# Kernel tuning notes

Measured on AMD Instinct MI355X. Metric: run time of the kernel, lower is better.

The kernel has to match this reference:

```python
import jax, jax.numpy as jnp
import numpy as np

EPS = 1e-5
LEAK = 0.01  # PADLoC uses ABN = BatchNorm + LeakyReLU as norm_act


def bn_act(x, g, b):
    # train-mode batch norm over (B,H,W) + leaky relu
    mu = jnp.mean(x, axis=(0, 2, 3), keepdims=True)
    var = jnp.var(x, axis=(0, 2, 3), keepdims=True)
    y = (x - mu) * jax.lax.rsqrt(var + EPS) * g[None, :, None, None] + b[None, :, None, None]
    return jnp.where(y >= 0, y, LEAK * y)


def depthwise3x3(x, w):
    # x: (B,C,H,W), w: (C,1,3,3), dilation (1,1), padding 1, groups=C
    C = x.shape[1]
    return jax.lax.conv_general_dilated(
        x, w, window_strides=(1, 1), padding=((1, 1), (1, 1)),
        feature_group_count=C, dimension_numbers=('NCHW', 'OIHW', 'NCHW'))


def pointwise(x, w):
    # 1x1 conv, no bias; w: (Cout, Cin)
    return jnp.einsum('bchw,oc->bohw', x, w)


def _gather_vals(x_flat, idx):
    # x_flat: (B,C,P), idx: (B,HW,9) float indices -> (B,C,HW,9)
    B, C, P = x_flat.shape
    i = idx.astype(jnp.int32).reshape(B, -1)  # (B, HW*9)
    out = jax.vmap(lambda xf, ii: xf[:, ii])(x_flat, i)  # (B,C,HW*9)
    return out.reshape(B, C, idx.shape[1], 9)


def setup_inputs() -> dict:
    key = jax.random.key(0)
    ks = jax.random.split(key, 8)
    B, Cin, Cout, H, W = 1, 256, 128, 64, 192
    sc = 0.05
    return {
        'x': jax.random.normal(ks[0], (B, Cin, H, W), jnp.float32),
        'x_range': jax.random.normal(ks[1], (B, 1, H, W), jnp.float32),
        'range_out': jax.random.normal(ks[2], (Cin, 1, 3, 3), jnp.float32) * sc,
        'w_reduce': jax.random.normal(ks[3], (Cout, Cin), jnp.float32) * sc,
        'g_r': jnp.ones((Cout,), jnp.float32), 'b_r': jnp.zeros((Cout,), jnp.float32),
        'dw1': jax.random.normal(ks[4], (Cout, 1, 3, 3), jnp.float32) * sc,
        'pw1': jax.random.normal(ks[5], (Cout, Cout), jnp.float32) * sc,
        'g1': jnp.ones((Cout,), jnp.float32), 'b1': jnp.zeros((Cout,), jnp.float32),
        'dw2': jax.random.normal(ks[6], (Cout, 1, 3, 3), jnp.float32) * sc,
        'pw2': jax.random.normal(ks[7], (Cout, Cout), jnp.float32) * sc,
        'g2': jnp.ones((Cout,), jnp.float32), 'b2': jnp.zeros((Cout,), jnp.float32),
    }


def reference(x, x_range, range_out, w_reduce, g_r, b_r, dw1, pw1, g1, b1, dw2, pw2, g2, b2):
    B, Cin, H, W = x.shape
    Hp, Wp = H + 2, W + 2
    P = Hp * Wp  # flattened padded spatial size
    x_off = jnp.array([-1, 0, 1, -1, 0, 1, -1, 0, 1], jnp.float32)
    y_off = jnp.array([-1, -1, -1, 0, 0, 0, 1, 1, 1], jnp.float32)

    offset = 3.0 * jax.nn.sigmoid(x_range)  # (B,1,H,W)

    # base (undeformed) flattened indices of the 9 taps around each interior pixel
    v = jnp.arange(P, dtype=jnp.float32)[:, None]  # (P,1)
    pre_v = v + x_off + y_off * Wp                 # (P,9)
    pre_v = pre_v.reshape(Hp, Wp, 9)[1:H + 1, 1:W + 1].reshape(-1, 9)  # (HW,9)
    pre_v = jnp.broadcast_to(pre_v[None], (B, H * W, 9))

    # fractional offsets: only x-direction is scaled by offset in _3x3box
    offset_v = offset.reshape(B, H * W, 1) * x_off.reshape(1, 1, 9) + (y_off * Wp).reshape(1, 1, 9)

    x_padded = jnp.pad(x, ((0, 0), (0, 0), (1, 1), (1, 1)))  # (B,C,Hp,Wp)
    clamp = lambda a: jnp.clip(a, 0.0, P - 1.0)

    after_v = pre_v + offset_v
    av_f = clamp(pre_v + jnp.floor(offset_v))
    av_f1 = clamp(av_f + x_off)
    av_c = clamp(pre_v + jnp.ceil(offset_v))
    av_c1 = clamp(av_c + x_off)

    xflat = x_padded.reshape(B, Cin, P)
    vf = _gather_vals(xflat, av_f)
    vf1 = _gather_vals(xflat, av_f1)
    vc = _gather_vals(xflat, av_c)
    vc1 = _gather_vals(xflat, av_c1)

    f1 = jnp.abs(after_v - av_f)[:, None] * vf + jnp.abs(av_f1 - after_v)[:, None] * vf1
    f2 = jnp.abs(after_v - av_c1)[:, None] * vc1 + jnp.abs(av_c - after_v)[:, None] * vc
    interp = (jnp.abs((after_v - av_f) / Wp)[:, None] * f1
              + jnp.abs((av_c1 - after_v) / Wp)[:, None] * f2)  # (B,C,HW,9)

    y = jnp.sum(interp * range_out.reshape(1, Cin, 1, 9), -1).reshape(B, Cin, H, W)
    y = bn_act(pointwise(y, w_reduce), g_r, b_r)
    y = bn_act(pointwise(depthwise3x3(y, dw1), pw1), g1, b1)
    y = bn_act(pointwise(depthwise3x3(y, dw2), pw2), g2, b2)
    return y
```

## Files before the change

### kernel.cpp

```cpp
#include <hip/hip_runtime.h>
#include <hip/hip_bf16.h>

#define HW    12288
#define Wimg  192
#define Himg  64
#define Wpad  194
#define Ppad  12804

static __device__ __forceinline__ unsigned short f2bf(float f) {
    union { float f; unsigned int u; } v; v.f = f;
    unsigned int r = v.u + 0x7fffu + ((v.u >> 16) & 1u);
    return (unsigned short)(r >> 16);
}
static __device__ __forceinline__ float bf2f(unsigned short h) {
    union { unsigned int u; float f; } v; v.u = ((unsigned int)h) << 16;
    return v.f;
}
static __device__ __forceinline__ float bflo(unsigned int u) {
    union { unsigned int u; float f; } v; v.u = u << 16; return v.f;
}
static __device__ __forceinline__ float bfhi(unsigned int u) {
    union { unsigned int u; float f; } v; v.u = u & 0xffff0000u; return v.f;
}

__global__ __launch_bounds__(256, 6) void k_deform(
    const float* __restrict__ x,
    const float* __restrict__ xr,
    const float* __restrict__ rout,
    unsigned short* __restrict__ y0)
{
    __shared__ unsigned short s_x[32][240];

    const int cblk = blockIdx.x;
    const int tile = blockIdx.y;
    const int tid  = threadIdx.x;
    const int pl   = tid & 63;
    const int wv   = __builtin_amdgcn_readfirstlane(tid >> 6);
    const int h    = tile / 3;
    const int w0   = (tile - h * 3) * 64;
    const int w    = w0 + pl;
    const int gp   = h * Wimg + w;

    int   li[6];
    float gw[6][3];
    const float off = 3.0f / (1.0f + expf(-xr[gp]));

    #pragma unroll
    for (int t = 0; t < 6; ++t) {
        const int xo = (t & 1) ? 1 : -1;
        const int yo = (t >> 1) - 1;
        float ov  = off * (float)xo;
        int   iv  = yo * Wpad;
        int   pre = (h + 1) * Wpad + (w + 1) + xo + iv;
        float after = (float)(pre + iv) + ov;
        int fl = (int)floorf(ov);
        int ce = (int)ceilf(ov);
        int av_f  = min(max(pre + fl + iv, 0), Ppad - 1);
        int av_f1 = min(max(av_f + xo,    0), Ppad - 1);
        int av_c  = min(max(pre + ce + iv, 0), Ppad - 1);
        int av_c1 = min(max(av_c + xo,    0), Ppad - 1);
        float wf  = fabsf(after - (float)av_f);
        float wf1 = fabsf((float)av_f1 - after);
        float wc1 = fabsf(after - (float)av_c1);
        float wc  = fabsf((float)av_c - after);
        float s1 = wf  * (1.0f / Wpad);
        float s2 = wc1 * (1.0f / Wpad);
        int   i4[4] = { av_f, av_f1, av_c1, av_c };
        float w4[4] = { s1 * wf, s1 * wf1, s2 * wc1, s2 * wc };
        int b = min(min(i4[0], i4[1]), min(i4[2], i4[3]));
        const int base = (h + 1 + 2 * yo) * Wpad + w0 - 4;
        li[t] = (t >> 1) * 80 + min(max(b - base, 0), 71);
        #pragma unroll
        for (int s = 0; s < 3; ++s) {
            float ws = 0.0f;
            #pragma unroll
            for (int j = 0; j < 4; ++j)
                ws += (i4[j] == b + s) ? w4[j] : 0.0f;
            int av = b + s;
            int r  = av / Wpad;
            int cc = av - r * Wpad;
            bool inb = (r >= 1) && (r <= Himg) && (cc >= 1) && (cc <= Wimg);
            gw[t][s] = inb ? ws : 0.0f;
        }
    }

    const int jj = tid;
    int  xoff = 0;
    bool valid = false;
    int  rr = 0, jcol = 0;
    if (jj < 222) {
        rr   = jj / 74;
        jcol = jj - rr * 74;
        const int flat = (h + 1 + 2 * (rr - 1)) * Wpad + w0 - 4 + jcol;
        if (flat >= 0 && flat < Ppad) {
            const int r = flat / Wpad;
            const int c = flat - r * Wpad;
            valid = (r >= 1) && (r <= Himg) && (c >= 1) && (c <= Wimg);
            xoff  = valid ? ((r - 1) * Wimg + (c - 1)) : 0;
        }
    }
    const float* xb = x + (size_t)(cblk * 32) * HW;
    for (int c = 0; c < 32; ++c) {
        if (jj < 222) {
            float v = valid ? xb[(size_t)c * HW + xoff] : 0.0f;
            s_x[c][rr * 80 + jcol] = f2bf(v);
        }
    }
    __syncthreads();

    const int c0l = wv * 8;
    #pragma unroll 2
    for (int i = 0; i < 8; ++i) {
        const int cl = c0l + i;
        const unsigned short* sxc = s_x[cl];
        const float* rc = rout + (cblk * 32 + cl) * 9;
        float acc = 0.0f;
        #pragma unroll
        for (int t = 0; t < 6; ++t) {
            float part = gw[t][0] * bf2f(sxc[li[t]])
                       + gw[t][1] * bf2f(sxc[li[t] + 1])
                       + gw[t][2] * bf2f(sxc[li[t] + 2]);
            const int k = 3 * (t >> 1) + ((t & 1) ? 2 : 0);
            acc += rc[k] * part;
        }
        y0[(size_t)(cblk * 32 + cl) * HW + gp] = f2bf(acc);
    }
}

template <int CIN>
__global__ __launch_bounds__(256) void k_pw(
    const unsigned short* __restrict__ A,
    const float* __restrict__ Wm,
    unsigned short* __restrict__ Zp0,
    unsigned short* __restrict__ Zp1)
{
    __shared__ float s_a[32][64];
    __shared__ float s_w[32][68];
    const int tid = threadIdx.x;
    const int tx  = tid & 15;
    const int ty  = tid >> 4;
    const int px0 = blockIdx.x * 64;
    const int o0  = blockIdx.y * 64;
    const int KH  = CIN / 2;
    const int cb0 = blockIdx.z * KH;
    unsigned short* __restrict__ Zp = blockIdx.z ? Zp1 : Zp0;

    float acc[4][4];
    #pragma unroll
    for (int i = 0; i < 4; ++i)
        #pragma unroll
        for (int j = 0; j < 4; ++j) acc[i][j] = 0.0f;

    const int arow = tid >> 3;
    const int acg  = tid & 7;
    const int wo = tid >> 5;
    const int wl = tid & 31;

    for (int cb = cb0; cb < cb0 + KH; cb += 32) {
        {
            const uint4* ap = (const uint4*)(A + (size_t)(cb + arow) * HW + px0);
            uint4 u = ap[acg];
            float4 lo = make_float4(bflo(u.x), bfhi(u.x), bflo(u.y), bfhi(u.y));
            float4 hi = make_float4(bflo(u.z), bfhi(u.z), bflo(u.w), bfhi(u.w));
            *(float4*)&s_a[arow][acg * 8]     = lo;
            *(float4*)&s_a[arow][acg * 8 + 4] = hi;
        }
        #pragma unroll
        for (int i = 0; i < 8; ++i)
            s_w[wl][wo + 8 * i] = Wm[(size_t)(o0 + wo + 8 * i) * CIN + cb + wl];
        __syncthreads();
        #pragma unroll
        for (int cc = 0; cc < 32; ++cc) {
            float4 a4 = *(const float4*)&s_a[cc][tx * 4];
            float4 w4 = *(const float4*)&s_w[cc][ty * 4];
            acc[0][0] += w4.x * a4.x; acc[0][1] += w4.x * a4.y;
            acc[0][2] += w4.x * a4.z; acc[0][3] += w4.x * a4.w;
            acc[1][0] += w4.y * a4.x; acc[1][1] += w4.y * a4.y;
            acc[1][2] += w4.y * a4.z; acc[1][3] += w4.y * a4.w;
            acc[2][0] += w4.z * a4.x; acc[2][1] += w4.z * a4.y;
            acc[2][2] += w4.z * a4.z; acc[2][3] += w4.z * a4.w;
            acc[3][0] += w4.w * a4.x; acc[3][1] += w4.w * a4.y;
            acc[3][2] += w4.w * a4.z; acc[3][3] += w4.w * a4.w;
        }
        __syncthreads();
    }

    #pragma unroll
    for (int i = 0; i < 4; ++i) {
        ushort4 v;
        v.x = f2bf(acc[i][0]); v.y = f2bf(acc[i][1]);
        v.z = f2bf(acc[i][2]); v.w = f2bf(acc[i][3]);
        *(ushort4*)&Zp[(size_t)(o0 + ty * 4 + i) * HW + px0 + tx * 4] = v;
    }
}

__global__ __launch_bounds__(256) void k_stats2(
    const unsigned short* __restrict__ Zp0,
    const unsigned short* __restrict__ Zp1,
    float* __restrict__ psum)
{
    __shared__ float s_s[4], s_q[4];
    const int c   = blockIdx.x;
    const int tid = threadIdx.x;
    const size_t base = (size_t)c * HW;
    const uint2* a4 = (const uint2*)(Zp0 + base);
    const uint2* b4 = (const uint2*)(Zp1 + base);
    float s = 0.0f, q = 0.0f;
    #pragma unroll
    for (int i = 0; i < 12; ++i) {
        uint2 a = a4[tid + i * 256];
        uint2 b = b4[tid + i * 256];
        float v0 = bflo(a.x) + bflo(b.x);
        float v1 = bfhi(a.x) + bfhi(b.x);
        float v2 = bflo(a.y) + bflo(b.y);
        float v3 = bfhi(a.y) + bfhi(b.y);
        s += v0 + v1 + v2 + v3;
        q += v0 * v0 + v1 * v1 + v2 * v2 + v3 * v3;
    }
    #pragma unroll
    for (int off = 32; off > 0; off >>= 1) {
        s += __shfl_down(s, off, 64);
        q += __shfl_down(q, off, 64);
    }
    if ((tid & 63) == 0) { s_s[tid >> 6] = s; s_q[tid >> 6] = q; }
    __syncthreads();
    if (tid == 0) {
        psum[2 * c]     = s_s[0] + s_s[1] + s_s[2] + s_s[3];
        psum[2 * c + 1] = s_q[0] + s_q[1] + s_q[2] + s_q[3];
    }
}

__global__ __launch_bounds__(256) void k_dw2(
    const unsigned short* __restrict__ Zp0,
    const unsigned short* __restrict__ Zp1,
    const float* __restrict__ psum,
    const float* __restrict__ g,
    const float* __restrict__ b,
    const float* __restrict__ dwgt,
    ushort4* __restrict__ D)
{
    const int t  = blockIdx.x * 256 + threadIdx.x;
    const int c  = t / 3072;
    const int gg = t - c * 3072;
    const int h  = gg / 48;
    const int w0 = (gg - h * 48) << 2;

    const float s   = psum[2 * c];
    const float q   = psum[2 * c + 1];
    const float mu  = s * (1.0f / HW);
    const float var = q * (1.0f / HW) - mu * mu;
    const float sc  = g[c] * rsqrtf(var + 1e-5f);
    const float sh  = b[c] - mu * sc;

    float wk[9];
    #pragma unroll
    for (int k = 0; k < 9; ++k) wk[k] = dwgt[c * 9 + k];

    const unsigned short* z0 = Zp0 + (size_t)c * HW;
    const unsigned short* z1 = Zp1 + (size_t)c * HW;
    float v[3][6];
    #pragma unroll
    for (int ky = 0; ky < 3; ++ky) {
        const int hh  = h + ky - 1;
        const bool rin = (hh >= 0) && (hh < Himg);
        #pragma unroll
        for (int j = 0; j < 6; ++j) {
            const int ww = w0 - 1 + j;
            const bool in = rin && (ww >= 0) && (ww < Wimg);
            float z = in ? (bf2f(z0[hh * Wimg + ww]) + bf2f(z1[hh * Wimg + ww]))
                         : 0.0f;
            float y = z * sc + sh;
            y = (y >= 0.0f) ? y : 0.01f * y;
            v[ky][j] = in ? y : 0.0f;
        }
    }

    ushort4 o;
    float oo[4];
    #pragma unroll
    for (int j = 0; j < 4; ++j) {
        float a = 0.0f;
        #pragma unroll
        for (int ky = 0; ky < 3; ++ky)
            #pragma unroll
            for (int kx = 0; kx < 3; ++kx)
                a += wk[ky * 3 + kx] * v[ky][j + kx];
        oo[j] = a;
    }
    o.x = f2bf(oo[0]); o.y = f2bf(oo[1]); o.z = f2bf(oo[2]); o.w = f2bf(oo[3]);
    D[t] = o;
}

__global__ __launch_bounds__(256) void k_final2(
    const unsigned short* __restrict__ Zp0,
    const unsigned short* __restrict__ Zp1,
    const float* __restrict__ psum,
    const float* __restrict__ g,
    const float* __restrict__ b,
    float4* __restrict__ out)
{
    const int f = blockIdx.x * 256 + threadIdx.x;
    const int c = f / 3072;

    const float s   = psum[2 * c];
    const float q   = psum[2 * c + 1];
    const float mu  = s * (1.0f / HW);
    const float var = q * (1.0f / HW) - mu * mu;
    const float sc  = g[c] * rsqrtf(var + 1e-5f);
    const float sh  = b[c] - mu * sc;

    uint2 a = ((const uint2*)Zp0)[f];
    uint2 d = ((const uint2*)Zp1)[f];
    float4 v;
    v.x = (bflo(a.x) + bflo(d.x)) * sc + sh; v.x = (v.x >= 0.0f) ? v.x : 0.01f * v.x;
    v.y = (bfhi(a.x) + bfhi(d.x)) * sc + sh; v.y = (v.y >= 0.0f) ? v.y : 0.01f * v.y;
    v.z = (bflo(a.y) + bflo(d.y)) * sc + sh; v.z = (v.z >= 0.0f) ? v.z : 0.01f * v.z;
    v.w = (bfhi(a.y) + bfhi(d.y)) * sc + sh; v.w = (v.w >= 0.0f) ? v.w : 0.01f * v.w;
    out[f] = v;
}

extern "C" void kernel_launch(void* const* d_in, const int* in_sizes, int n_in,
                              void* d_out, int out_size, void* d_ws, size_t ws_size,
                              hipStream_t stream) {
    const float* x   = (const float*)d_in[0];
    const float* xr  = (const float*)d_in[1];
    const float* ro  = (const float*)d_in[2];
    const float* wr  = (const float*)d_in[3];
    const float* gr  = (const float*)d_in[4];
    const float* br  = (const float*)d_in[5];
    const float* dw1 = (const float*)d_in[6];
    const float* pw1 = (const float*)d_in[7];
    const float* g1  = (const float*)d_in[8];
    const float* b1  = (const float*)d_in[9];
    const float* dw2 = (const float*)d_in[10];
    const float* pw2 = (const float*)d_in[11];
    const float* g2  = (const float*)d_in[12];
    const float* b2  = (const float*)d_in[13];

    unsigned short* WS = (unsigned short*)d_ws;
    unsigned short* y0  = WS;
    unsigned short* D   = WS;
    unsigned short* P0a = WS + 3145728;
    unsigned short* P0b = WS + 4718592;
    unsigned short* P1a = WS + 6291456;
    unsigned short* P1b = WS + 7864320;
    float* p1 = (float*)(WS + 9437184);
    float* p2 = p1 + 256;
    float* p3 = p2 + 256;
    float* out = (float*)d_out;

    k_deform<<<dim3(8, 192), 256, 0, stream>>>(x, xr, ro, y0);
    k_pw<256><<<dim3(192, 2, 2), 256, 0, stream>>>(y0, wr, P0a, P0b);
    k_stats2<<<128, 256, 0, stream>>>(P0a, P0b, p1);
    k_dw2<<<1536, 256, 0, stream>>>(P0a, P0b, p1, gr, br, dw1, (ushort4*)D);
    k_pw<128><<<dim3(192, 2, 2), 256, 0, stream>>>(D, pw1, P1a, P1b);
    k_stats2<<<128, 256, 0, stream>>>(P1a, P1b, p2);
    k_dw2<<<1536, 256, 0, stream>>>(P1a, P1b, p2, g1, b1, dw2, (ushort4*)D);
    k_pw<128><<<dim3(192, 2, 2), 256, 0, stream>>>(D, pw2, P0a, P0b);
    k_stats2<<<128, 256, 0, stream>>>(P0a, P0b, p3);
    k_final2<<<1536, 256, 0, stream>>>(P0a, P0b, p3, g2, b2, (float4*)out);
}
```

Baseline: 168.7 us.

## Use bf16 MFMA pointwise convs with fused BN stats via atomics

Replaces the FP32 SIMT 1x1-conv GEMM with MFMA 16x16x32 bf16 instructions. Weights are split into hi/lo bf16 pairs to keep near-fp32 precision, and the activation tile is staged in swizzled LDS. Per-channel sum and sum-of-squares are accumulated in the GEMM epilogue with wave shuffles and atomics, which removes the separate stats kernels and the split-K partial buffers. This cuts launches and memory traffic, at the cost of atomic contention, doubled MFMA work for the split weights, and nondeterministic reduction order.

Result: slower. 416.1 us (+146.6%).

```diff
diff --git a/kernel.cpp b/kernel.cpp
--- a/kernel.cpp
+++ b/kernel.cpp
@@ -1,5 +1,4 @@
 #include <hip/hip_runtime.h>
-#include <hip/hip_bf16.h>
 
 #define HW    12288
 #define Wimg  192
@@ -7,6 +6,9 @@
 #define Wpad  194
 #define Ppad  12804
 
+typedef __attribute__((ext_vector_type(8))) __bf16 bf16x8;
+typedef __attribute__((ext_vector_type(4))) float  f32x4;
+
 static __device__ __forceinline__ unsigned short f2bf(float f) {
     union { float f; unsigned int u; } v; v.f = f;
     unsigned int r = v.u + 0x7fffu + ((v.u >> 16) & 1u);
@@ -22,14 +24,24 @@
 static __device__ __forceinline__ float bfhi(unsigned int u) {
     union { unsigned int u; float f; } v; v.u = u & 0xffff0000u; return v.f;
 }
+static __device__ __forceinline__ __bf16 us2bf(unsigned short u) {
+    union { unsigned short u; __bf16 b; } v; v.u = u; return v.b;
+}
 
 __global__ __launch_bounds__(256, 6) void k_deform(
     const float* __restrict__ x,
     const float* __restrict__ xr,
     const float* __restrict__ rout,
-    unsigned short* __restrict__ y0)
+    unsigned short* __restrict__ y0,
+    float* __restrict__ psz)
 {
     __shared__ unsigned short s_x[32][240];
+
+    if (blockIdx.x == 0 && blockIdx.y == 0) {
+        psz[threadIdx.x]       = 0.0f;
+        psz[threadIdx.x + 256] = 0.0f;
+        psz[threadIdx.x + 512] = 0.0f;
+    }
 
     const int cblk = blockIdx.x;
     const int tile = blockIdx.y;
@@ -128,111 +140,97 @@
 }
 
 template <int CIN>
-__global__ __launch_bounds__(256) void k_pw(
-    const unsigned short* __restrict__ A,
+__global__ __launch_bounds__(256) void k_pw_mfma(
+    const unsigned short* __restrict__ Aact,
     const float* __restrict__ Wm,
-    unsigned short* __restrict__ Zp0,
-    unsigned short* __restrict__ Zp1)
-{
-    __shared__ float s_a[32][64];
-    __shared__ float s_w[32][68];
-    const int tid = threadIdx.x;
-    const int tx  = tid & 15;
-    const int ty  = tid >> 4;
-    const int px0 = blockIdx.x * 64;
-    const int o0  = blockIdx.y * 64;
-    const int KH  = CIN / 2;
-    const int cb0 = blockIdx.z * KH;
-    unsigned short* __restrict__ Zp = blockIdx.z ? Zp1 : Zp0;
-
-    float acc[4][4];
-    #pragma unroll
-    for (int i = 0; i < 4; ++i)
-        #pragma unroll
-        for (int j = 0; j < 4; ++j) acc[i][j] = 0.0f;
-
-    const int arow = tid >> 3;
-    const int acg  = tid & 7;
-    const int wo = tid >> 5;
-    const int wl = tid & 31;
-
-    for (int cb = cb0; cb < cb0 + KH; cb += 32) {
-        {
-            const uint4* ap = (const uint4*)(A + (size_t)(cb + arow) * HW + px0);
-            uint4 u = ap[acg];
-            float4 lo = make_float4(bflo(u.x), bfhi(u.x), bflo(u.y), bfhi(u.y));
-            float4 hi = make_float4(bflo(u.z), bfhi(u.z), bflo(u.w), bfhi(u.w));
-            *(float4*)&s_a[arow][acg * 8]     = lo;
-            *(float4*)&s_a[arow][acg * 8 + 4] = hi;
-        }
-        #pragma unroll
-        for (int i = 0; i < 8; ++i)
-            s_w[wl][wo + 8 * i] = Wm[(size_t)(o0 + wo + 8 * i) * CIN + cb + wl];
-        __syncthreads();
-        #pragma unroll
-        for (int cc = 0; cc < 32; ++cc) {
-            float4 a4 = *(const float4*)&s_a[cc][tx * 4];
-            float4 w4 = *(const float4*)&s_w[cc][ty * 4];
-            acc[0][0] += w4.x * a4.x; acc[0][1] += w4.x * a4.y;
-            acc[0][2] += w4.x * a4.z; acc[0][3] += w4.x * a4.w;
-            acc[1][0] += w4.y * a4.x; acc[1][1] += w4.y * a4.y;
-            acc[1][2] += w4.y * a4.z; acc[1][3] += w4.y * a4.w;
-            acc[2][0] += w4.z * a4.x; acc[2][1] += w4.z * a4.y;
-            acc[2][2] += w4.z * a4.z; acc[2][3] += w4.z * a4.w;
-            acc[3][0] += w4.w * a4.x; acc[3][1] += w4.w * a4.y;
-            acc[3][2] += w4.w * a4.z; acc[3][3] += w4.w * a4.w;
-        }
-        __syncthreads();
-    }
-
-    #pragma unroll
-    for (int i = 0; i < 4; ++i) {
-        ushort4 v;
-        v.x = f2bf(acc[i][0]); v.y = f2bf(acc[i][1]);
-        v.z = f2bf(acc[i][2]); v.w = f2bf(acc[i][3]);
-        *(ushort4*)&Zp[(size_t)(o0 + ty * 4 + i) * HW + px0 + tx * 4] = v;
-    }
-}
-
-__global__ __launch_bounds__(256) void k_stats2(
-    const unsigned short* __restrict__ Zp0,
-    const unsigned short* __restrict__ Zp1,
+    unsigned short* __restrict__ Z,
     float* __restrict__ psum)
 {
-    __shared__ float s_s[4], s_q[4];
-    const int c   = blockIdx.x;
+    constexpr int KC = CIN / 32;
+    constexpr int RS = CIN + 8;
+    __shared__ __align__(16) unsigned short s_b[32][RS];
+
     const int tid = threadIdx.x;
-    const size_t base = (size_t)c * HW;
-    const uint2* a4 = (const uint2*)(Zp0 + base);
-    const uint2* b4 = (const uint2*)(Zp1 + base);
-    float s = 0.0f, q = 0.0f;
-    #pragma unroll
-    for (int i = 0; i < 12; ++i) {
-        uint2 a = a4[tid + i * 256];
-        uint2 b = b4[tid + i * 256];
-        float v0 = bflo(a.x) + bflo(b.x);
-        float v1 = bfhi(a.x) + bfhi(b.x);
-        float v2 = bflo(a.y) + bflo(b.y);
-        float v3 = bfhi(a.y) + bfhi(b.y);
-        s += v0 + v1 + v2 + v3;
-        q += v0 * v0 + v1 * v1 + v2 * v2 + v3 * v3;
-    }
-    #pragma unroll
-    for (int off = 32; off > 0; off >>= 1) {
-        s += __shfl_down(s, off, 64);
-        q += __shfl_down(q, off, 64);
-    }
-    if ((tid & 63) == 0) { s_s[tid >> 6] = s; s_q[tid >> 6] = q; }
+    const int l   = tid & 63;
+    const int wv  = tid >> 6;
+    const int px0 = blockIdx.x * 32;
+    const int o0  = blockIdx.y * 64;
+
+    {
+        const int cs  = tid >> 1;
+        const int pxb = (tid & 1) << 4;
+        const int swz = (tid & 1) << 3;
+        #pragma unroll
+        for (int it = 0; it < CIN / 128; ++it) {
+            const int c = cs + it * 128;
+            const uint4* src = (const uint4*)(Aact + (size_t)c * HW + px0 + pxb);
+            uint4 u0 = src[0];
+            uint4 u1 = src[1];
+            const int sc = c ^ swz;
+            unsigned int wd[8] = {u0.x, u0.y, u0.z, u0.w, u1.x, u1.y, u1.z, u1.w};
+            #pragma unroll
+            for (int e = 0; e < 8; ++e) {
+                s_b[pxb + 2 * e    ][sc] = (unsigned short)(wd[e] & 0xffffu);
+                s_b[pxb + 2 * e + 1][sc] = (unsigned short)(wd[e] >> 16);
+            }
+        }
+    }
+
+    bf16x8 wh[KC], wl[KC];
+    {
+        const int orow = o0 + wv * 16 + (l & 15);
+        const float* wp = Wm + (size_t)orow * CIN + ((l >> 4) << 3);
+        #pragma unroll
+        for (int kc = 0; kc < KC; ++kc) {
+            #pragma unroll
+            for (int j = 0; j < 8; ++j) {
+                float f = wp[kc * 32 + j];
+                unsigned short hu = f2bf(f);
+                unsigned short lu = f2bf(f - bf2f(hu));
+                wh[kc][j] = us2bf(hu);
+                wl[kc][j] = us2bf(lu);
+            }
+        }
+    }
     __syncthreads();
-    if (tid == 0) {
-        psum[2 * c]     = s_s[0] + s_s[1] + s_s[2] + s_s[3];
-        psum[2 * c + 1] = s_q[0] + s_q[1] + s_q[2] + s_q[3];
-    }
-}
-
-__global__ __launch_bounds__(256) void k_dw2(
-    const unsigned short* __restrict__ Zp0,
-    const unsigned short* __restrict__ Zp1,
+
+    f32x4 acc[2] = { {0.f, 0.f, 0.f, 0.f}, {0.f, 0.f, 0.f, 0.f} };
+    const int prow = l & 15;
+    const int kg8  = l >> 4;
+    #pragma unroll
+    for (int kc = 0; kc < KC; ++kc) {
+        #pragma unroll
+        for (int ip = 0; ip < 2; ++ip) {
+            const int col = kc * 32 + (((kg8 ^ ip) & 3) << 3);
+            bf16x8 bfr = *(const bf16x8*)&s_b[ip * 16 + prow][col];
+            acc[ip] = __builtin_amdgcn_mfma_f32_16x16x32_bf16(wh[kc], bfr, acc[ip], 0, 0, 0);
+            acc[ip] = __builtin_amdgcn_mfma_f32_16x16x32_bf16(wl[kc], bfr, acc[ip], 0, 0, 0);
+        }
+    }
+
+    const int obase = o0 + wv * 16 + ((l >> 4) << 2);
+    #pragma unroll
+    for (int r = 0; r < 4; ++r) {
+        const int ch = obase + r;
+        float v0 = acc[0][r];
+        float v1 = acc[1][r];
+        Z[(size_t)ch * HW + px0 + prow]      = f2bf(v0);
+        Z[(size_t)ch * HW + px0 + 16 + prow] = f2bf(v1);
+        float s = v0 + v1;
+        float q = v0 * v0 + v1 * v1;
+        s += __shfl_xor(s, 1, 64);  q += __shfl_xor(q, 1, 64);
+        s += __shfl_xor(s, 2, 64);  q += __shfl_xor(q, 2, 64);
+        s += __shfl_xor(s, 4, 64);  q += __shfl_xor(q, 4, 64);
+        s += __shfl_xor(s, 8, 64);  q += __shfl_xor(q, 8, 64);
+        if (prow == 0) {
+            atomicAdd(&psum[2 * ch],     s);
+            atomicAdd(&psum[2 * ch + 1], q);
+        }
+    }
+}
+
+__global__ __launch_bounds__(256) void k_dw(
+    const unsigned short* __restrict__ Zs,
     const float* __restrict__ psum,
     const float* __restrict__ g,
     const float* __restrict__ b,
@@ -256,8 +254,7 @@
     #pragma unroll
     for (int k = 0; k < 9; ++k) wk[k] = dwgt[c * 9 + k];
 
-    const unsigned short* z0 = Zp0 + (size_t)c * HW;
-    const unsigned short* z1 = Zp1 + (size_t)c * HW;
+    const unsigned short* z0 = Zs + (size_t)c * HW;
     float v[3][6];
     #pragma unroll
     for (int ky = 0; ky < 3; ++ky) {
@@ -267,8 +264,7 @@
         for (int j = 0; j < 6; ++j) {
             const int ww = w0 - 1 + j;
             const bool in = rin && (ww >= 0) && (ww < Wimg);
-            float z = in ? (bf2f(z0[hh * Wimg + ww]) + bf2f(z1[hh * Wimg + ww]))
-                         : 0.0f;
+            float z = in ? bf2f(z0[hh * Wimg + ww]) : 0.0f;
             float y = z * sc + sh;
             y = (y >= 0.0f) ? y : 0.01f * y;
             v[ky][j] = in ? y : 0.0f;
@@ -291,9 +287,8 @@
     D[t] = o;
 }
 
-__global__ __launch_bounds__(256) void k_final2(
-    const unsigned short* __restrict__ Zp0,
-    const unsigned short* __restrict__ Zp1,
+__global__ __launch_bounds__(256) void k_final(
+    const unsigned short* __restrict__ Zs,
     const float* __restrict__ psum,
     const float* __restrict__ g,
     const float* __restrict__ b,
@@ -309,13 +304,12 @@
     const float sc  = g[c] * rsqrtf(var + 1e-5f);
     const float sh  = b[c] - mu * sc;
 
-    uint2 a = ((const uint2*)Zp0)[f];
-    uint2 d = ((const uint2*)Zp1)[f];
+    uint2 a = ((const uint2*)Zs)[f];
     float4 v;
-    v.x = (bflo(a.x) + bflo(d.x)) * sc + sh; v.x = (v.x >= 0.0f) ? v.x : 0.01f * v.x;
-    v.y = (bfhi(a.x) + bfhi(d.x)) * sc + sh; v.y = (v.y >= 0.0f) ? v.y : 0.01f * v.y;
-    v.z = (bflo(a.y) + bflo(d.y)) * sc + sh; v.z = (v.z >= 0.0f) ? v.z : 0.01f * v.z;
-    v.w = (bfhi(a.y) + bfhi(d.y)) * sc + sh; v.w = (v.w >= 0.0f) ? v.w : 0.01f * v.w;
+    v.x = bflo(a.x) * sc + sh; v.x = (v.x >= 0.0f) ? v.x : 0.01f * v.x;
+    v.y = bfhi(a.x) * sc + sh; v.y = (v.y >= 0.0f) ? v.y : 0.01f * v.y;
+    v.z = bflo(a.y) * sc + sh; v.z = (v.z >= 0.0f) ? v.z : 0.01f * v.z;
+    v.w = bfhi(a.y) * sc + sh; v.w = (v.w >= 0.0f) ? v.w : 0.01f * v.w;
     out[f] = v;
 }
 
@@ -338,25 +332,21 @@
     const float* b2  = (const float*)d_in[13];
 
     unsigned short* WS = (unsigned short*)d_ws;
-    unsigned short* y0  = WS;
-    unsigned short* D   = WS;
-    unsigned short* P0a = WS + 3145728;
-    unsigned short* P0b = WS + 4718592;
-    unsigned short* P1a = WS + 6291456;
-    unsigned short* P1b = WS + 7864320;
+    unsigned short* y0 = WS;
+    unsigned short* Z1 = WS + 3145728;
+    unsigned short* D  = WS + 4718592;
+    unsigned short* Z2 = WS + 6291456;
+    unsigned short* Z3 = WS + 7864320;
     float* p1 = (float*)(WS + 9437184);
     float* p2 = p1 + 256;
     float* p3 = p2 + 256;
     float* out = (float*)d_out;
 
-    k_deform<<<dim3(8, 192), 256, 0, stream>>>(x, xr, ro, y0);
-    k_pw<256><<<dim3(192, 2, 2), 256, 0, stream>>>(y0, wr, P0a, P0b);
-    k_stats2<<<128, 256, 0, stream>>>(P0a, P0b, p1);
-    k_dw2<<<1536, 256, 0, stream>>>(P0a, P0b, p1, gr, br, dw1, (ushort4*)D);
-    k_pw<128><<<dim3(192, 2, 2), 256, 0, stream>>>(D, pw1, P1a, P1b);
-    k_stats2<<<128, 256, 0, stream>>>(P1a, P1b, p2);
-    k_dw2<<<1536, 256, 0, stream>>>(P1a, P1b, p2, g1, b1, dw2, (ushort4*)D);
-    k_pw<128><<<dim3(192, 2, 2), 256, 0, stream>>>(D, pw2, P0a, P0b);
-    k_stats2<<<128, 256, 0, stream>>>(P0a, P0b, p3);
-    k_final2<<<1536, 256, 0, stream>>>(P0a, P0b, p3, g2, b2, (float4*)out);
-}
+    k_deform<<<dim3(8, 192), 256, 0, stream>>>(x, xr, ro, y0, p1);
+    k_pw_mfma<256><<<dim3(384, 2), 256, 0, stream>>>(y0, wr, Z1, p1);
+    k_dw<<<1536, 256, 0, stream>>>(Z1, p1, gr, br, dw1, (ushort4*)D);
+    k_pw_mfma<128><<<dim3(384, 2), 256, 0, stream>>>(D, pw1, Z2, p2);
+    k_dw<<<1536, 256, 0, stream>>>(Z2, p2, g1, b1, dw2, (ushort4*)D);
+    k_pw_mfma<128><<<dim3(384, 2), 256, 0, stream>>>(D, pw2, Z3, p3);
+    k_final<<<1536, 256, 0, stream>>>(Z3, p3, g2, b2, (float4*)out);
+}
```
